# Optimization experiments

Measured on AMD Instinct MI355X. Metric: run time of the kernel, lower is better.

## Reference

```python
import jax, jax.numpy as jnp
import numpy as np


def _compute_gradient(f, src, dst, egw):
    # f: [b, c, n] node features; src/dst: [b, e] edge endpoints; egw: [b, e, d]
    # gradient at node src = sum_edges pinvdx * (f[dst] - f[src])
    fT = f.transpose(0, 2, 1)  # b, n, c
    n = fT.shape[1]
    f_dst = jnp.take_along_axis(fT, dst[..., None], axis=1)  # b, e, c
    f_src = jnp.take_along_axis(fT, src[..., None], axis=1)  # b, e, c
    msg = egw[..., :, None] * (f_dst - f_src)[..., None, :]  # b, e, d, c
    b, e, d, c = msg.shape

    def seg(m, s):
        return jax.ops.segment_sum(m.reshape(e, d * c), s, num_segments=n)

    grad = jax.vmap(seg)(msg, src)  # b, n, d*c
    return grad.transpose(0, 2, 1)  # b, d*c, n


def _forward(x, t, nodes, node_weights, edge_gradient_weights, modes, sp_L,
             fc0_w, fc0_b, Wc, Ws, W0, ws_w, ws_b, gws_w, gws_b,
             fc1_w, fc1_b, fc2_w, fc2_b, directed_edges):
    D = nodes.shape[-1]
    # Fourier bases: modes [k,d,w] scaled by sp_L [d,w]
    temp = jnp.einsum('bxd,kdw->bxkw', nodes, modes * sp_L)
    bc, bs = jnp.cos(temp), jnp.sin(temp)
    b0 = jnp.ones(temp[:, :, :1, :].shape, temp.dtype)
    nw = node_weights[:, :, None, :]
    wbc, wbs, wb0 = bc * nw, bs * nw, b0 * nw

    x_value = x[:, :, :D]
    h = jnp.concatenate([x, t], -1) @ fc0_w + fc0_b  # b, n, c
    h = h.transpose(0, 2, 1)  # b, c, n

    src = directed_edges[..., 0]
    dst = directed_edges[..., 1]
    nlayers = ws_w.shape[0]
    for i in range(nlayers):
        # spectral convolution (real Fourier transform on scattered points)
        xc = jnp.einsum('bcx,bxkw->bckw', h, wbc)
        xs = -jnp.einsum('bcx,bxkw->bckw', h, wbs)
        x0 = jnp.einsum('bcx,bxkw->bckw', h, wb0)
        fc_ = jnp.einsum('bikw,iokw->bokw', xc, Wc[i]) - jnp.einsum('bikw,iokw->bokw', xs, Ws[i])
        fs_ = jnp.einsum('bikw,iokw->bokw', xs, Wc[i]) + jnp.einsum('bikw,iokw->bokw', xc, Ws[i])
        f0_ = jnp.einsum('bikw,iokw->bokw', x0, W0[i])
        x1 = (jnp.einsum('bokw,bxkw->box', f0_, b0)
              + 2.0 * jnp.einsum('bokw,bxkw->box', fc_, bc)
              - 2.0 * jnp.einsum('bokw,bxkw->box', fs_, bs))
        # pointwise linear (Conv1d kernel size 1)
        x2 = jnp.einsum('oc,bcx->box', ws_w[i], h) + ws_b[i][None, :, None]
        # gradient operator + softsign + Conv1d
        g = _compute_gradient(h, src, dst, edge_gradient_weights)  # b, d*c, n
        g = g / (1.0 + jnp.abs(g))  # softsign
        x3 = jnp.einsum('oc,bcx->box', gws_w[i], g) + gws_b[i][None, :, None]
        h = x1 + x2 + x3
        if i != nlayers - 1:
            h = jax.nn.gelu(h, approximate=False)

    h = h.transpose(0, 2, 1)  # b, n, c
    h = jax.nn.gelu(h @ fc1_w + fc1_b, approximate=False)
    h = h @ fc2_w + fc2_b
    return x_value + t * h


def setup_inputs() -> dict:
    B, N, E = 2, 20000, 100000
    D, W, K, C, L, FC, OUT = 3, 1, 128, 128, 3, 128, 3
    key = jax.random.key(0)
    k = jax.random.split(key, 16)
    x = jax.random.normal(k[0], (B, N, D), jnp.float32)
    t = jax.random.uniform(k[1], (B, N, 1), jnp.float32)
    node_mask = jnp.ones((B, N, 1), jnp.int32)
    nodes = jax.random.uniform(k[2], (B, N, D), jnp.float32)
    node_weights = jax.random.uniform(k[3], (B, N, W), jnp.float32) / N
    directed_edges = jax.random.randint(k[4], (B, E, 2), 0, N)
    edge_gradient_weights = jax.random.normal(k[5], (B, E, D), jnp.float32)
    modes = jax.random.normal(k[6], (K, D, W), jnp.float32) * (2.0 * np.pi)
    sp_L = jnp.ones((D, W), jnp.float32)
    fc0_w = jax.random.normal(k[7], (D + 1, C), jnp.float32) * 0.1
    fc0_b = jnp.zeros((C,), jnp.float32)
    scale = 1.0 / (C * C)
    Wc = jax.random.uniform(k[8], (L, C, C, K, W), jnp.float32) * scale
    Ws = jax.random.uniform(k[9], (L, C, C, K, W), jnp.float32) * scale
    W0 = jax.random.uniform(k[10], (L, C, C, 1, W), jnp.float32) * scale
    ws_w = jax.random.normal(k[11], (L, C, C), jnp.float32) * 0.05
    ws_b = jnp.zeros((L, C), jnp.float32)
    gws_w = jax.random.normal(k[12], (L, C, D * C), jnp.float32) * 0.05
    gws_b = jnp.zeros((L, C), jnp.float32)
    fc1_w = jax.random.normal(k[13], (C, FC), jnp.float32) * 0.05
    fc1_b = jnp.zeros((FC,), jnp.float32)
    fc2_w = jax.random.normal(k[14], (FC, OUT), jnp.float32) * 0.05
    fc2_b = jnp.zeros((OUT,), jnp.float32)
    return dict(x=x, t=t, node_mask=node_mask, nodes=nodes, node_weights=node_weights,
                directed_edges=directed_edges, edge_gradient_weights=edge_gradient_weights,
                modes=modes, sp_L=sp_L, fc0_w=fc0_w, fc0_b=fc0_b, Wc=Wc, Ws=Ws, W0=W0,
                ws_w=ws_w, ws_b=ws_b, gws_w=gws_w, gws_b=gws_b,
                fc1_w=fc1_w, fc1_b=fc1_b, fc2_w=fc2_w, fc2_b=fc2_b)


def reference(x, t, node_mask, nodes, node_weights, directed_edges, edge_gradient_weights,
              modes, sp_L, fc0_w, fc0_b, Wc, Ws, W0, ws_w, ws_b, gws_w, gws_b,
              fc1_w, fc1_b, fc2_w, fc2_b):
    del node_mask  # unpacked but unused in the original forward
    return _forward(x, t, nodes, node_weights, edge_gradient_weights, modes, sp_L,
                    fc0_w, fc0_b, Wc, Ws, W0, ws_w, ws_b, gws_w, gws_b,
                    fc1_w, fc1_b, fc2_w, fc2_b, directed_edges)
```

## Files before the change

### kernel.cpp

```cpp
#include <hip/hip_runtime.h>
#include <math.h>

#define BB 2
#define NN 20000
#define EE 100000
#define DD 3
#define KK 128
#define CC 128
#define LL 3
#define FCC 128
#define GJ (DD*CC)
#define KR 768
#define NP 20096
#define NCHK 157
#define G1CH 79
#define G1N 256

typedef __attribute__((ext_vector_type(8))) short bf16x8;
typedef __attribute__((ext_vector_type(4))) float f32x4;

__device__ inline unsigned short f2bf(float f) {
  unsigned int u = __float_as_uint(f);
  u += 0x7fffu + ((u >> 16) & 1u);
  return (unsigned short)(u >> 16);
}
__device__ inline float bf2f(unsigned short u) {
  return __uint_as_float(((unsigned int)u) << 16);
}

__device__ float d_nw[BB*NN];
__device__ __align__(16) unsigned short d_stackT[(size_t)BB*NP*KR];
__device__ __align__(16) unsigned short d_bcT[(size_t)BB*KK*NP];
__device__ __align__(16) unsigned short d_bsT[(size_t)BB*KK*NP];
__device__ __align__(16) unsigned short d_hTwT[(size_t)BB*CC*NP];
__device__ __align__(16) unsigned short d_uTb[(size_t)BB*NP*FCC];
__device__ __align__(16) unsigned short d_Amatb[BB*CC*KR];
__device__ __align__(16) unsigned short d_fc1wb[FCC*CC];
__device__ __align__(16) float d_part[(size_t)BB*4*G1CH*2*64*64];
__device__ float d_xc[BB*CC*KK];
__device__ float d_xs[BB*CC*KK];
__device__ float d_x0p[BB*NCHK*CC];
__device__ float d_fcp[BB*CC*8*KK];
__device__ float d_fsp[BB*CC*8*KK];
__device__ float d_bias[BB*CC];
__device__ int d_cnt[BB*NN];
__device__ int d_cursor[BB*NN];
__device__ int d_off[BB*(NN+1)];
__device__ __align__(16) float4 d_erec[(size_t)BB*EE];

__global__ __launch_bounds__(128) void k_basis(const float* __restrict__ nodes,
                                               const float* __restrict__ nodew,
                                               const float* __restrict__ modes,
                                               const float* __restrict__ spL) {
  int bn = blockIdx.x;
  int k  = threadIdx.x;
  int b = bn / NN, n = bn % NN;
  float x0 = nodes[bn*3+0], x1 = nodes[bn*3+1], x2 = nodes[bn*3+2];
  float tmp = x0*modes[k*3+0]*spL[0] + x1*modes[k*3+1]*spL[1] + x2*modes[k*3+2]*spL[2];
  float cv = cosf(tmp), sv = sinf(tmp);
  size_t row = (size_t)(b*NP + n);
  d_stackT[row*KR + k]       = f2bf(cv);
  d_stackT[row*KR + 128 + k] = f2bf(sv);
  if (k == 0) d_nw[bn] = nodew[bn];
}

__global__ __launch_bounds__(256) void k_basisT() {
  __shared__ unsigned short t1[32][136];
  __shared__ unsigned short t2[32][136];
  int blk = blockIdx.x;
  int nt = blk % 628, b = blk / 628;
  int n0 = nt*32;
  int tid = threadIdx.x;
  int kl = tid & 127, ng = tid >> 7;
  for (int nn = ng; nn < 32; nn += 2) {
    int n = n0 + nn;
    unsigned short cv = 0, sv = 0;
    if (n < NN) {
      const unsigned short* sp = d_stackT + ((size_t)(b*NP + n))*KR;
      cv = sp[kl]; sv = sp[128 + kl];
    }
    t1[nn][kl] = cv;
    t2[nn][kl] = sv;
  }
  __syncthreads();
  int nl = tid & 31, kg = tid >> 5;
  for (int k = kg; k < 128; k += 8) {
    d_bcT[((size_t)(b*KK + k))*NP + n0 + nl] = t1[nl][k];
    d_bsT[((size_t)(b*KK + k))*NP + n0 + nl] = t2[nl][k];
  }
}

__global__ __launch_bounds__(256) void k_csr_zero() {
  int tid = blockIdx.x*256 + threadIdx.x;
  if (tid < BB*NN) { d_cnt[tid] = 0; d_cursor[tid] = 0; }
}

__global__ __launch_bounds__(256) void k_csr_count(const int* __restrict__ edges) {
  int e = blockIdx.x*256 + threadIdx.x;
  if (e >= BB*EE) return;
  int b = e / EE;
  int src = edges[e*2 + 0];
  atomicAdd(&d_cnt[b*NN + src], 1);
}

__global__ __launch_bounds__(1024) void k_csr_scan() {
  int b = blockIdx.x;
  __shared__ int sdata[1024];
  __shared__ int carry_s;
  int tid = threadIdx.x;
  if (tid == 0) carry_s = 0;
  __syncthreads();
  for (int chunk = 0; chunk < 20; ++chunk) {
    int i = chunk*1024 + tid;
    int v = (i < NN) ? d_cnt[b*NN + i] : 0;
    sdata[tid] = v;
    __syncthreads();
    for (int s = 1; s < 1024; s <<= 1) {
      int tv = (tid >= s) ? sdata[tid - s] : 0;
      __syncthreads();
      sdata[tid] += tv;
      __syncthreads();
    }
    int excl = carry_s + sdata[tid] - v;
    if (i < NN) d_off[b*(NN+1) + i] = excl;
    __syncthreads();
    if (tid == 1023) carry_s += sdata[1023];
    __syncthreads();
  }
  if (tid == 0) d_off[b*(NN+1) + NN] = carry_s;
}

__global__ __launch_bounds__(256) void k_csr_scatter(const int* __restrict__ edges,
                                                     const float* __restrict__ egw) {
  int e = blockIdx.x*256 + threadIdx.x;
  if (e >= BB*EE) return;
  int b = e / EE;
  int src = edges[e*2 + 0];
  int dst = edges[e*2 + 1];
  int pos = atomicAdd(&d_cursor[b*NN + src], 1);
  d_erec[(size_t)b*EE + d_off[b*(NN+1) + src] + pos] =
      make_float4(__int_as_float(dst), egw[e*3+0], egw[e*3+1], egw[e*3+2]);
}

__global__ __launch_bounds__(256) void k_h0(const float* __restrict__ x,
                                            const float* __restrict__ t,
                                            const float* __restrict__ w,
                                            const float* __restrict__ bias) {
  int tid = blockIdx.x*256 + threadIdx.x;
  int c = tid & 127;
  int bn = tid >> 7;
  int b = bn / NN, n = bn % NN;
  const float* xv = x + bn*3;
  float acc = bias[c] + xv[0]*w[c] + xv[1]*w[CC+c] + xv[2]*w[2*CC+c]
            + t[bn]*w[3*CC+c];
  d_stackT[((size_t)(b*NP + n))*KR + 256 + c] = f2bf(acc);
}

__global__ __launch_bounds__(256) void k_hT0() {
  __shared__ unsigned short t[128][136];
  int chunk = blockIdx.x;
  int b = blockIdx.y;
  int n0 = chunk*128;
  int tid = threadIdx.x;
  int cl = tid & 127, ng = tid >> 7;
  for (int nn = ng; nn < 128; nn += 2) {
    int n = n0 + nn;
    unsigned short v = 0;
    if (n < NN) {
      float hv = bf2f(d_stackT[((size_t)(b*NP + n))*KR + 256 + cl]);
      v = f2bf(hv * d_nw[b*NN + n]);
    }
    t[nn][cl] = v;
  }
  __syncthreads();
  int nl = tid & 31, cg = tid >> 5;
  for (int c = cg; c < 128; c += 8)
    for (int nn2 = 0; nn2 < 128; nn2 += 32)
      d_hTwT[((size_t)(b*CC + c))*NP + n0 + nn2 + nl] = t[nn2 + nl][c];
}

__global__ __launch_bounds__(256) void k_gemm1m() {
  __shared__ unsigned short Ash[2][64*40];
  __shared__ unsigned short Bch[2][64*40];
  __shared__ unsigned short Bsh[2][64*40];
  int chunk = blockIdx.x;
  int quad  = blockIdx.y;
  int b     = blockIdx.z;
  int ch = quad >> 1, kh = quad & 1;
  int tid = threadIdx.x, lane = tid & 63, wid = tid >> 6;
  int q = lane >> 4, m = lane & 15;
  f32x4 accC[4], accS[4];
  #pragma unroll
  for (int j = 0; j < 4; j++) { accC[j] = (f32x4){0.f,0.f,0.f,0.f}; accS[j] = (f32x4){0.f,0.f,0.f,0.f}; }
  const unsigned short* Ab  = d_hTwT + ((size_t)(b*CC + ch*64))*NP;
  const unsigned short* Bcp = d_bcT + ((size_t)(b*KK + kh*64))*NP;
  const unsigned short* Bsp = d_bsT + ((size_t)(b*KK + kh*64))*NP;
  int n0 = chunk*G1N;

#define G1STAGE(nb, d) { \
    int row_ = tid >> 2; int e8_ = (tid & 3)*8; \
    if ((nb) < NP) { \
      *(uint4*)&Ash[d][row_*40 + e8_] = *(const uint4*)(Ab  + (size_t)row_*NP + (nb) + e8_); \
      *(uint4*)&Bch[d][row_*40 + e8_] = *(const uint4*)(Bcp + (size_t)row_*NP + (nb) + e8_); \
      *(uint4*)&Bsh[d][row_*40 + e8_] = *(const uint4*)(Bsp + (size_t)row_*NP + (nb) + e8_); \
    } else { \
      uint4 z_ = make_uint4(0,0,0,0); \
      *(uint4*)&Ash[d][row_*40 + e8_] = z_; \
      *(uint4*)&Bch[d][row_*40 + e8_] = z_; \
      *(uint4*)&Bsh[d][row_*40 + e8_] = z_; \
    } }

  G1STAGE(n0, 0)
  int cur = 0;
  for (int s = 0; s < G1N/32; s++) {
    __syncthreads();
    if (s + 1 < G1N/32) G1STAGE(n0 + (s+1)*32, cur ^ 1)
    bf16x8 a = *(const bf16x8*)&Ash[cur][(wid*16 + m)*40 + q*8];
    #pragma unroll
    for (int kt = 0; kt < 4; kt++) {
      bf16x8 bcf = *(const bf16x8*)&Bch[cur][(kt*16 + m)*40 + q*8];
      accC[kt] = __builtin_amdgcn_mfma_f32_16x16x32_bf16(a, bcf, accC[kt], 0, 0, 0);
      bf16x8 bsf = *(const bf16x8*)&Bsh[cur][(kt*16 + m)*40 + q*8];
      accS[kt] = __builtin_amdgcn_mfma_f32_16x16x32_bf16(a, bsf, accS[kt], 0, 0, 0);
    }
    cur ^= 1;
  }
#undef G1STAGE

  float* base = d_part + ((size_t)(b*4 + quad)*G1CH + chunk)*2*4096;
  #pragma unroll
  for (int kt = 0; kt < 4; kt++)
    #pragma unroll
    for (int r = 0; r < 4; r++) {
      int c = wid*16 + q*4 + r;
      int k = kt*16 + m;
      base[c*64 + k]        =  accC[kt][r];
      base[4096 + c*64 + k] = -accS[kt][r];
    }
}

__global__ __launch_bounds__(256) void k_red_x0() {
  int blk = blockIdx.x;
  if (blk < 256) {
    int tid = blk*256 + threadIdx.x;
    int k = tid & 127;
    int c = (tid >> 7) & 127;
    int arr = (tid >> 14) & 1;
    int b = tid >> 15;
    int ch = c >> 6, cl = c & 63;
    int kh = k >> 6, kl = k & 63;
    int quad = ch*2 + kh;
    const float* p = d_part + ((size_t)(b*4 + quad)*G1CH)*2*4096 + arr*4096 + cl*64 + kl;
    float acc = 0.f;
    for (int t = 0; t < G1CH; t++) acc += p[(size_t)t*2*4096];
    if (arr == 0) d_xc[(b*CC + c)*KK + k] = acc;
    else          d_xs[(b*CC + c)*KK + k] = acc;
  } else {
    int bc = blk - 256;
    int chunk = bc % NCHK, b = bc / NCHK;
    int tid = threadIdx.x;
    int c = tid >> 1, half = tid & 1;
    const unsigned short* p = d_hTwT + ((size_t)(b*CC + c))*NP + chunk*128 + half*64;
    float acc = 0.f;
    #pragma unroll
    for (int i = 0; i < 8; i++) {
      ushort4 v0 = *(const ushort4*)&p[i*8];
      ushort4 v1 = *(const ushort4*)&p[i*8 + 4];
      acc += bf2f(v0.x) + bf2f(v0.y) + bf2f(v0.z) + bf2f(v0.w)
           + bf2f(v1.x) + bf2f(v1.y) + bf2f(v1.z) + bf2f(v1.w);
    }
    __shared__ float red[128][2];
    red[c][half] = acc;
    __syncthreads();
    if (half == 0) d_x0p[(b*NCHK + chunk)*CC + c] = red[c][0] + red[c][1];
  }
}

__global__ __launch_bounds__(128) void k_spec(const float* __restrict__ Wc,
                                              const float* __restrict__ Ws, int l) {
  int bo = blockIdx.x;
  int ch = blockIdx.y;
  int b = bo >> 7;
  int o = bo & 127;
  int k = threadIdx.x;
  int i0 = ch*16;
  const float* wcp = Wc + ((size_t)(l*CC + i0)*CC + o)*KK + k;
  const float* wsp = Ws + ((size_t)(l*CC + i0)*CC + o)*KK + k;
  float fc = 0.f, fs = 0.f;
  #pragma unroll 4
  for (int j = 0; j < 16; j++) {
    int i = i0 + j;
    float xcv = d_xc[(b*CC + i)*KK + k];
    float xsv = d_xs[(b*CC + i)*KK + k];
    float wcv = wcp[(size_t)j*CC*KK];
    float wsv = wsp[(size_t)j*CC*KK];
    fc += xcv*wcv - xsv*wsv;
    fs += xsv*wcv + xcv*wsv;
  }
  d_fcp[((size_t)bo*8 + ch)*KK + k] = fc;
  d_fsp[((size_t)bo*8 + ch)*KK + k] = fs;
}

__global__ __launch_bounds__(128) void k_bA_f0(const float* __restrict__ wsw,
                                               const float* __restrict__ gwsw,
                                               const float* __restrict__ W0,
                                               const float* __restrict__ wsb,
                                               const float* __restrict__ gwsb, int l) {
  int blk = blockIdx.x;
  int t = threadIdx.x;
  if (blk < 256) {
    int bo = blk;
    int b = bo >> 7, o = bo & 127;
    float fc = 0.f, fs = 0.f;
    #pragma unroll
    for (int ch = 0; ch < 8; ch++) {
      fc += d_fcp[((size_t)bo*8 + ch)*KK + t];
      fs += d_fsp[((size_t)bo*8 + ch)*KK + t];
    }
    unsigned short* dst = d_Amatb + (size_t)bo*KR;
    dst[t]       = f2bf( 2.f*fc);
    dst[128 + t] = f2bf(-2.f*fs);
    dst[256 + t] = f2bf(wsw[(l*CC + o)*CC + t]);
    #pragma unroll
    for (int j = 0; j < 3; j++)
      dst[384 + j*128 + t] = f2bf(gwsw[(size_t)(l*CC + o)*GJ + j*128 + t]);
  } else {
    int b = blk - 256;
    int o = t;
    __shared__ float sx[CC];
    float xv = 0.f;
    for (int p = 0; p < NCHK; p++) xv += d_x0p[(b*NCHK + p)*CC + o];
    sx[o] = xv;
    __syncthreads();
    float acc = 0.f;
    for (int i = 0; i < CC; i++) acc += sx[i]*W0[(l*CC + i)*CC + o];
    d_bias[b*CC + o] = acc + wsb[l*CC + o] + gwsb[l*CC + o];
  }
}

__global__ __launch_bounds__(128) void k_fc1w(const float* __restrict__ fc1w) {
  int c = blockIdx.x;
  int o2 = threadIdx.x;
  d_fc1wb[o2*CC + c] = f2bf(fc1w[c*FCC + o2]);
}

__global__ __launch_bounds__(128) void k_grad_csr() {
  int bn = blockIdx.x;
  int b = bn / NN, n = bn % NN;
  int c = threadIdx.x;
  int beg = d_off[b*(NN+1) + n];
  int end = d_off[b*(NN+1) + n + 1];
  const float4* rp = d_erec + (size_t)b*EE;
  const unsigned short* hb = d_stackT + (size_t)b*NP*KR + 256 + c;
  float a0 = 0.f, a1 = 0.f, a2 = 0.f;
  float sw0 = 0.f, sw1 = 0.f, sw2 = 0.f;
  int p = beg;
  for (; p + 4 <= end; p += 4) {
    float4 r1 = rp[p], r2 = rp[p+1], r3 = rp[p+2], r4 = rp[p+3];
    float f1 = bf2f(hb[(size_t)__float_as_int(r1.x)*KR]);
    float f2 = bf2f(hb[(size_t)__float_as_int(r2.x)*KR]);
    float f3 = bf2f(hb[(size_t)__float_as_int(r3.x)*KR]);
    float f4 = bf2f(hb[(size_t)__float_as_int(r4.x)*KR]);
    a0 += r1.y*f1 + r2.y*f2 + r3.y*f3 + r4.y*f4;
    a1 += r1.z*f1 + r2.z*f2 + r3.z*f3 + r4.z*f4;
    a2 += r1.w*f1 + r2.w*f2 + r3.w*f3 + r4.w*f4;
    sw0 += r1.y + r2.y + r3.y + r4.y;
    sw1 += r1.z + r2.z + r3.z + r4.z;
    sw2 += r1.w + r2.w + r3.w + r4.w;
  }
  for (; p < end; ++p) {
    float4 r1 = rp[p];
    float f1 = bf2f(hb[(size_t)__float_as_int(r1.x)*KR]);
    a0 += r1.y*f1; a1 += r1.z*f1; a2 += r1.w*f1;
    sw0 += r1.y; sw1 += r1.z; sw2 += r1.w;
  }
  float fs = bf2f(hb[(size_t)n*KR]);
  a0 -= sw0*fs; a1 -= sw1*fs; a2 -= sw2*fs;
  unsigned short* gp = d_stackT + ((size_t)(b*NP + n))*KR + 384;
  gp[c]        = f2bf(a0/(1.f + fabsf(a0)));
  gp[CC + c]   = f2bf(a1/(1.f + fabsf(a1)));
  gp[2*CC + c] = f2bf(a2/(1.f + fabsf(a2)));
}

__global__ __launch_bounds__(512) void k_mfma(int koff, int K,
                                              const unsigned short* __restrict__ W, size_t wstride,
                                              unsigned short* __restrict__ OutB,
                                              const float* __restrict__ bias, int bias_stride,
                                              int gelu, int aux) {
  __shared__ unsigned short As[2][64*72];
  __shared__ unsigned short Bs[2][128*72];
  __shared__ float sh_nw[64];
  int b = blockIdx.z;
  int n_base = blockIdx.x*64;
  int tid = threadIdx.x;
  int lane = tid & 63, wid = tid >> 6;
  int wr = wid >> 1, wc = wid & 1;
  int q = lane >> 4, m = lane & 15;

  f32x4 acc[4];
  #pragma unroll
  for (int j = 0; j < 4; j++) acc[j] = (f32x4){0.f,0.f,0.f,0.f};

  const unsigned short* Wb = W + (size_t)b*wstride;
  const unsigned short* Ab = d_stackT + (size_t)b*NP*KR + koff;

#define STAGE(k0, d) { \
    { int rowA = tid >> 3; int e8A = (tid & 7)*8; \
      *(uint4*)&As[d][rowA*72 + e8A] = *(const uint4*)(Ab + (size_t)(n_base + rowA)*KR + (k0) + e8A); } \
    _Pragma("unroll") \
    for (int i_ = 0; i_ < 2; i_++) { \
      int idx_ = tid + i_*512; int rowB = idx_ >> 3; int e8B = (idx_ & 7)*8; \
      *(uint4*)&Bs[d][rowB*72 + e8B] = *(const uint4*)(Wb + (size_t)rowB*K + (k0) + e8B); } }

  STAGE(0, 0)
  int cur = 0;
  for (int k0 = 0; k0 < K; k0 += 64) {
    __syncthreads();
    if (k0 + 64 < K) STAGE(k0 + 64, cur ^ 1)
    bf16x8 a0 = *(const bf16x8*)&As[cur][(wr*16 + m)*72 + q*8];
    bf16x8 a1 = *(const bf16x8*)&As[cur][(wr*16 + m)*72 + 32 + q*8];
    #pragma unroll
    for (int ot = 0; ot < 4; ot++) {
      bf16x8 b0 = *(const bf16x8*)&Bs[cur][(wc*64 + ot*16 + m)*72 + q*8];
      acc[ot] = __builtin_amdgcn_mfma_f32_16x16x32_bf16(a0, b0, acc[ot], 0, 0, 0);
      bf16x8 b1 = *(const bf16x8*)&Bs[cur][(wc*64 + ot*16 + m)*72 + 32 + q*8];
      acc[ot] = __builtin_amdgcn_mfma_f32_16x16x32_bf16(a1, b1, acc[ot], 0, 0, 0);
    }
    cur ^= 1;
  }
#undef STAGE

  __syncthreads();
  unsigned short* Ep = &As[0][0];
  if (tid < 64) {
    int n = n_base + tid;
    sh_nw[tid] = (aux && n < NN) ? d_nw[b*NN + n] : 0.f;
  }
  const float* bp = bias + (size_t)b*bias_stride;
  int lrow = wr*16 + q*4;
  #pragma unroll
  for (int ot = 0; ot < 4; ot++) {
    int o = wc*64 + ot*16 + m;
    float bvv = bp[o];
    #pragma unroll
    for (int r = 0; r < 4; r++) {
      float v = acc[ot][r] + bvv;
      if (gelu) v = 0.5f*v*(1.f + erff(v*0.70710678118f));
      Ep[(lrow + r)*132 + o] = f2bf(v);
    }
  }
  __syncthreads();
  {
    int row = tid >> 3;
    int c16 = (tid & 7)*16;
    int n = n_base + row;
    uint4 v0 = *(uint4*)&Ep[row*132 + c16];
    uint4 v1 = *(uint4*)&Ep[row*132 + c16 + 8];
    if (aux) {
      if (n < NN) {
        unsigned short* dst = d_stackT + ((size_t)(b*NP + n))*KR + 256;
        *(uint4*)&dst[c16]     = v0;
        *(uint4*)&dst[c16 + 8] = v1;
      }
    } else {
      unsigned short* dst = OutB + ((size_t)(b*NP + n))*FCC;
      *(uint4*)&dst[c16]     = v0;
      *(uint4*)&dst[c16 + 8] = v1;
    }
  }
  if (aux) {
    int o = tid >> 2;
    int j0 = (tid & 3)*16;
    unsigned short tmp[16];
    #pragma unroll
    for (int j = 0; j < 16; j++) {
      float hv = bf2f(Ep[(j0 + j)*132 + o]);
      tmp[j] = f2bf(hv * sh_nw[j0 + j]);
    }
    unsigned short* dst = d_hTwT + ((size_t)(b*CC + o))*NP + n_base + j0;
    *(uint4*)&dst[0] = *(uint4*)&tmp[0];
    *(uint4*)&dst[8] = *(uint4*)&tmp[8];
  }
}

__global__ __launch_bounds__(256) void k_out(const float* __restrict__ x,
                                             const float* __restrict__ t,
                                             const float* __restrict__ fc2w,
                                             const float* __restrict__ fc2b,
                                             float* __restrict__ out) {
  int tid = blockIdx.x*256 + threadIdx.x;
  if (tid >= BB*NN) return;
  int b = tid / NN, n = tid % NN;
  const unsigned short* up = d_uTb + ((size_t)(b*NP + n))*FCC;
  float a0 = fc2b[0], a1 = fc2b[1], a2v = fc2b[2];
  #pragma unroll 4
  for (int o2 = 0; o2 < FCC; o2 += 4) {
    ushort4 uv = *(const ushort4*)&up[o2];
    float u0 = bf2f(uv.x), u1 = bf2f(uv.y), u2 = bf2f(uv.z), u3 = bf2f(uv.w);
    a0  += u0*fc2w[(o2+0)*3+0] + u1*fc2w[(o2+1)*3+0] + u2*fc2w[(o2+2)*3+0] + u3*fc2w[(o2+3)*3+0];
    a1  += u0*fc2w[(o2+0)*3+1] + u1*fc2w[(o2+1)*3+1] + u2*fc2w[(o2+2)*3+1] + u3*fc2w[(o2+3)*3+1];
    a2v += u0*fc2w[(o2+0)*3+2] + u1*fc2w[(o2+1)*3+2] + u2*fc2w[(o2+2)*3+2] + u3*fc2w[(o2+3)*3+2];
  }
  float tv = t[tid];
  out[tid*3 + 0] = x[tid*3 + 0] + tv*a0;
  out[tid*3 + 1] = x[tid*3 + 1] + tv*a1;
  out[tid*3 + 2] = x[tid*3 + 2] + tv*a2v;
}

extern "C" void kernel_launch(void* const* d_in, const int* in_sizes, int n_in,
                              void* d_out, int out_size, void* d_ws, size_t ws_size,
                              hipStream_t stream) {
  const float* x     = (const float*)d_in[0];
  const float* t     = (const float*)d_in[1];
  const float* nodes = (const float*)d_in[3];
  const float* nodew = (const float*)d_in[4];
  const int*   edges = (const int*)d_in[5];
  const float* egw   = (const float*)d_in[6];
  const float* modes = (const float*)d_in[7];
  const float* spL   = (const float*)d_in[8];
  const float* fc0w  = (const float*)d_in[9];
  const float* fc0b  = (const float*)d_in[10];
  const float* Wc    = (const float*)d_in[11];
  const float* Ws    = (const float*)d_in[12];
  const float* W0    = (const float*)d_in[13];
  const float* wsw   = (const float*)d_in[14];
  const float* wsb   = (const float*)d_in[15];
  const float* gwsw  = (const float*)d_in[16];
  const float* gwsb  = (const float*)d_in[17];
  const float* fc1w  = (const float*)d_in[18];
  const float* fc1b  = (const float*)d_in[19];
  const float* fc2w  = (const float*)d_in[20];
  const float* fc2b  = (const float*)d_in[21];
  float* out = (float*)d_out;

  unsigned short* d_Amatb_p; hipGetSymbolAddress((void**)&d_Amatb_p, HIP_SYMBOL(d_Amatb));
  unsigned short* d_fc1wb_p; hipGetSymbolAddress((void**)&d_fc1wb_p, HIP_SYMBOL(d_fc1wb));
  unsigned short* d_uTb_p;   hipGetSymbolAddress((void**)&d_uTb_p,   HIP_SYMBOL(d_uTb));
  float* d_bias_p;  hipGetSymbolAddress((void**)&d_bias_p,  HIP_SYMBOL(d_bias));

  hipLaunchKernelGGL(k_basis, dim3(BB*NN), dim3(128), 0, stream, nodes, nodew, modes, spL);
  hipLaunchKernelGGL(k_basisT, dim3(628*BB), dim3(256), 0, stream);
  hipLaunchKernelGGL(k_h0, dim3(BB*NN*CC/256), dim3(256), 0, stream, x, t, fc0w, fc0b);
  hipLaunchKernelGGL(k_hT0, dim3(NCHK, BB), dim3(256), 0, stream);
  hipLaunchKernelGGL(k_fc1w, dim3(CC), dim3(FCC), 0, stream, fc1w);
  hipLaunchKernelGGL(k_csr_zero, dim3((BB*NN + 255)/256), dim3(256), 0, stream);
  hipLaunchKernelGGL(k_csr_count, dim3((BB*EE + 255)/256), dim3(256), 0, stream, edges);
  hipLaunchKernelGGL(k_csr_scan, dim3(BB), dim3(1024), 0, stream);
  hipLaunchKernelGGL(k_csr_scatter, dim3((BB*EE + 255)/256), dim3(256), 0, stream, edges, egw);

  for (int l = 0; l < LL; l++) {
    hipLaunchKernelGGL(k_gemm1m, dim3(G1CH, 4, BB), dim3(256), 0, stream);
    hipLaunchKernelGGL(k_red_x0, dim3(256 + NCHK*BB), dim3(256), 0, stream);
    hipLaunchKernelGGL(k_spec, dim3(BB*CC, 8), dim3(128), 0, stream, Wc, Ws, l);
    hipLaunchKernelGGL(k_bA_f0, dim3(BB*CC + BB), dim3(128), 0, stream,
                       wsw, gwsw, W0, wsb, gwsb, l);
    hipLaunchKernelGGL(k_grad_csr, dim3(BB*NN), dim3(128), 0, stream);
    hipLaunchKernelGGL(k_mfma, dim3(NP/64, 1, BB), dim3(512), 0, stream,
                       0, KR, d_Amatb_p, (size_t)CC*KR, d_uTb_p, d_bias_p, CC,
                       (l != LL-1) ? 1 : 0, 1);
  }

  hipLaunchKernelGGL(k_mfma, dim3(NP/64, 1, BB), dim3(512), 0, stream,
                     256, CC, d_fc1wb_p, (size_t)0, d_uTb_p, fc1b, 0, 1, 0);
  hipLaunchKernelGGL(k_out, dim3((BB*NN + 255)/256), dim3(256), 0, stream, x, t, fc2w, fc2b, out);
}
```

Measured before the change: 495.0 us.

## Co-schedule spectral GEMM with gradient kernel and fuse fc2 output into final GEMM

The spectral partial GEMM and the CSR gradient gather are merged into one launch with disjoint block ranges, so the memory-bound gather can run alongside the MFMA work. The GEMM also drops LDS double buffering in favour of a single buffer with two barriers per step. The fc2 projection and residual output move into the epilogue of the final fc1 MFMA kernel, which removes the intermediate bf16 activation buffer and one launch. The single-buffered loop exposes load latency, and the combined kernel's block mix may be scheduled unevenly.

```diff
diff --git a/kernel.cpp b/kernel.cpp
--- a/kernel.cpp
+++ b/kernel.cpp
@@ -15,6 +15,7 @@
 #define NCHK 157
 #define G1CH 79
 #define G1N 256
+#define G1BLK (G1CH*4*BB)
 
 typedef __attribute__((ext_vector_type(8))) short bf16x8;
 typedef __attribute__((ext_vector_type(4))) float f32x4;
@@ -33,7 +34,6 @@
 __device__ __align__(16) unsigned short d_bcT[(size_t)BB*KK*NP];
 __device__ __align__(16) unsigned short d_bsT[(size_t)BB*KK*NP];
 __device__ __align__(16) unsigned short d_hTwT[(size_t)BB*CC*NP];
-__device__ __align__(16) unsigned short d_uTb[(size_t)BB*NP*FCC];
 __device__ __align__(16) unsigned short d_Amatb[BB*CC*KR];
 __device__ __align__(16) unsigned short d_fc1wb[FCC*CC];
 __device__ __align__(16) float d_part[(size_t)BB*4*G1CH*2*64*64];
@@ -179,64 +179,100 @@
       d_hTwT[((size_t)(b*CC + c))*NP + n0 + nn2 + nl] = t[nn2 + nl][c];
 }
 
-__global__ __launch_bounds__(256) void k_gemm1m() {
-  __shared__ unsigned short Ash[2][64*40];
-  __shared__ unsigned short Bch[2][64*40];
-  __shared__ unsigned short Bsh[2][64*40];
-  int chunk = blockIdx.x;
-  int quad  = blockIdx.y;
-  int b     = blockIdx.z;
-  int ch = quad >> 1, kh = quad & 1;
-  int tid = threadIdx.x, lane = tid & 63, wid = tid >> 6;
-  int q = lane >> 4, m = lane & 15;
-  f32x4 accC[4], accS[4];
-  #pragma unroll
-  for (int j = 0; j < 4; j++) { accC[j] = (f32x4){0.f,0.f,0.f,0.f}; accS[j] = (f32x4){0.f,0.f,0.f,0.f}; }
-  const unsigned short* Ab  = d_hTwT + ((size_t)(b*CC + ch*64))*NP;
-  const unsigned short* Bcp = d_bcT + ((size_t)(b*KK + kh*64))*NP;
-  const unsigned short* Bsp = d_bsT + ((size_t)(b*KK + kh*64))*NP;
-  int n0 = chunk*G1N;
-
-#define G1STAGE(nb, d) { \
-    int row_ = tid >> 2; int e8_ = (tid & 3)*8; \
-    if ((nb) < NP) { \
-      *(uint4*)&Ash[d][row_*40 + e8_] = *(const uint4*)(Ab  + (size_t)row_*NP + (nb) + e8_); \
-      *(uint4*)&Bch[d][row_*40 + e8_] = *(const uint4*)(Bcp + (size_t)row_*NP + (nb) + e8_); \
-      *(uint4*)&Bsh[d][row_*40 + e8_] = *(const uint4*)(Bsp + (size_t)row_*NP + (nb) + e8_); \
-    } else { \
-      uint4 z_ = make_uint4(0,0,0,0); \
-      *(uint4*)&Ash[d][row_*40 + e8_] = z_; \
-      *(uint4*)&Bch[d][row_*40 + e8_] = z_; \
-      *(uint4*)&Bsh[d][row_*40 + e8_] = z_; \
-    } }
-
-  G1STAGE(n0, 0)
-  int cur = 0;
-  for (int s = 0; s < G1N/32; s++) {
-    __syncthreads();
-    if (s + 1 < G1N/32) G1STAGE(n0 + (s+1)*32, cur ^ 1)
-    bf16x8 a = *(const bf16x8*)&Ash[cur][(wid*16 + m)*40 + q*8];
-    #pragma unroll
-    for (int kt = 0; kt < 4; kt++) {
-      bf16x8 bcf = *(const bf16x8*)&Bch[cur][(kt*16 + m)*40 + q*8];
-      accC[kt] = __builtin_amdgcn_mfma_f32_16x16x32_bf16(a, bcf, accC[kt], 0, 0, 0);
-      bf16x8 bsf = *(const bf16x8*)&Bsh[cur][(kt*16 + m)*40 + q*8];
-      accS[kt] = __builtin_amdgcn_mfma_f32_16x16x32_bf16(a, bsf, accS[kt], 0, 0, 0);
-    }
-    cur ^= 1;
-  }
-#undef G1STAGE
-
-  float* base = d_part + ((size_t)(b*4 + quad)*G1CH + chunk)*2*4096;
-  #pragma unroll
-  for (int kt = 0; kt < 4; kt++)
-    #pragma unroll
-    for (int r = 0; r < 4; r++) {
-      int c = wid*16 + q*4 + r;
-      int k = kt*16 + m;
-      base[c*64 + k]        =  accC[kt][r];
-      base[4096 + c*64 + k] = -accS[kt][r];
-    }
+__global__ __launch_bounds__(256) void k_g1grad() {
+  __shared__ unsigned short Ash[64*40];
+  __shared__ unsigned short Bch[64*40];
+  __shared__ unsigned short Bsh[64*40];
+  int blk = blockIdx.x;
+  int tid = threadIdx.x;
+
+  if (blk < G1BLK) {
+    int chunk = blk % G1CH;
+    int quad  = (blk / G1CH) & 3;
+    int b     = blk / (G1CH*4);
+    int ch = quad >> 1, kh = quad & 1;
+    int lane = tid & 63, wid = tid >> 6;
+    int q = lane >> 4, m = lane & 15;
+    f32x4 accC[4], accS[4];
+    #pragma unroll
+    for (int j = 0; j < 4; j++) { accC[j] = (f32x4){0.f,0.f,0.f,0.f}; accS[j] = (f32x4){0.f,0.f,0.f,0.f}; }
+    const unsigned short* Ab  = d_hTwT + ((size_t)(b*CC + ch*64))*NP;
+    const unsigned short* Bcp = d_bcT + ((size_t)(b*KK + kh*64))*NP;
+    const unsigned short* Bsp = d_bsT + ((size_t)(b*KK + kh*64))*NP;
+    int n0 = chunk*G1N;
+    for (int s = 0; s < G1N/32; s++) {
+      int nb = n0 + s*32;
+      __syncthreads();
+      {
+        int row_ = tid >> 2; int e8_ = (tid & 3)*8;
+        if (nb < NP) {
+          *(uint4*)&Ash[row_*40 + e8_] = *(const uint4*)(Ab  + (size_t)row_*NP + nb + e8_);
+          *(uint4*)&Bch[row_*40 + e8_] = *(const uint4*)(Bcp + (size_t)row_*NP + nb + e8_);
+          *(uint4*)&Bsh[row_*40 + e8_] = *(const uint4*)(Bsp + (size_t)row_*NP + nb + e8_);
+        } else {
+          uint4 z_ = make_uint4(0,0,0,0);
+          *(uint4*)&Ash[row_*40 + e8_] = z_;
+          *(uint4*)&Bch[row_*40 + e8_] = z_;
+          *(uint4*)&Bsh[row_*40 + e8_] = z_;
+        }
+      }
+      __syncthreads();
+      bf16x8 a = *(const bf16x8*)&Ash[(wid*16 + m)*40 + q*8];
+      #pragma unroll
+      for (int kt = 0; kt < 4; kt++) {
+        bf16x8 bcf = *(const bf16x8*)&Bch[(kt*16 + m)*40 + q*8];
+        accC[kt] = __builtin_amdgcn_mfma_f32_16x16x32_bf16(a, bcf, accC[kt], 0, 0, 0);
+        bf16x8 bsf = *(const bf16x8*)&Bsh[(kt*16 + m)*40 + q*8];
+        accS[kt] = __builtin_amdgcn_mfma_f32_16x16x32_bf16(a, bsf, accS[kt], 0, 0, 0);
+      }
+    }
+    float* base = d_part + ((size_t)(b*4 + quad)*G1CH + chunk)*2*4096;
+    #pragma unroll
+    for (int kt = 0; kt < 4; kt++)
+      #pragma unroll
+      for (int r = 0; r < 4; r++) {
+        int c = wid*16 + q*4 + r;
+        int k = kt*16 + m;
+        base[c*64 + k]        =  accC[kt][r];
+        base[4096 + c*64 + k] = -accS[kt][r];
+      }
+  } else {
+    int bn = (blk - G1BLK)*2 + (tid >> 7);
+    int c = tid & 127;
+    int b = bn / NN, n = bn % NN;
+    int beg = d_off[b*(NN+1) + n];
+    int end = d_off[b*(NN+1) + n + 1];
+    const float4* rp = d_erec + (size_t)b*EE;
+    const unsigned short* hb = d_stackT + (size_t)b*NP*KR + 256 + c;
+    float a0 = 0.f, a1 = 0.f, a2 = 0.f;
+    float sw0 = 0.f, sw1 = 0.f, sw2 = 0.f;
+    int p = beg;
+    for (; p + 4 <= end; p += 4) {
+      float4 r1 = rp[p], r2 = rp[p+1], r3 = rp[p+2], r4 = rp[p+3];
+      float f1 = bf2f(hb[(size_t)__float_as_int(r1.x)*KR]);
+      float f2 = bf2f(hb[(size_t)__float_as_int(r2.x)*KR]);
+      float f3 = bf2f(hb[(size_t)__float_as_int(r3.x)*KR]);
+      float f4 = bf2f(hb[(size_t)__float_as_int(r4.x)*KR]);
+      a0 += r1.y*f1 + r2.y*f2 + r3.y*f3 + r4.y*f4;
+      a1 += r1.z*f1 + r2.z*f2 + r3.z*f3 + r4.z*f4;
+      a2 += r1.w*f1 + r2.w*f2 + r3.w*f3 + r4.w*f4;
+      sw0 += r1.y + r2.y + r3.y + r4.y;
+      sw1 += r1.z + r2.z + r3.z + r4.z;
+      sw2 += r1.w + r2.w + r3.w + r4.w;
+    }
+    for (; p < end; ++p) {
+      float4 r1 = rp[p];
+      float f1 = bf2f(hb[(size_t)__float_as_int(r1.x)*KR]);
+      a0 += r1.y*f1; a1 += r1.z*f1; a2 += r1.w*f1;
+      sw0 += r1.y; sw1 += r1.z; sw2 += r1.w;
+    }
+    float fs = bf2f(hb[(size_t)n*KR]);
+    a0 -= sw0*fs; a1 -= sw1*fs; a2 -= sw2*fs;
+    unsigned short* gp = d_stackT + ((size_t)(b*NP + n))*KR + 384;
+    gp[c]        = f2bf(a0/(1.f + fabsf(a0)));
+    gp[CC + c]   = f2bf(a1/(1.f + fabsf(a1)));
+    gp[2*CC + c] = f2bf(a2/(1.f + fabsf(a2)));
+  }
 }
 
 __global__ __launch_bounds__(256) void k_red_x0() {
@@ -344,49 +380,15 @@
   d_fc1wb[o2*CC + c] = f2bf(fc1w[c*FCC + o2]);
 }
 
-__global__ __launch_bounds__(128) void k_grad_csr() {
-  int bn = blockIdx.x;
-  int b = bn / NN, n = bn % NN;
-  int c = threadIdx.x;
-  int beg = d_off[b*(NN+1) + n];
-  int end = d_off[b*(NN+1) + n + 1];
-  const float4* rp = d_erec + (size_t)b*EE;
-  const unsigned short* hb = d_stackT + (size_t)b*NP*KR + 256 + c;
-  float a0 = 0.f, a1 = 0.f, a2 = 0.f;
-  float sw0 = 0.f, sw1 = 0.f, sw2 = 0.f;
-  int p = beg;
-  for (; p + 4 <= end; p += 4) {
-    float4 r1 = rp[p], r2 = rp[p+1], r3 = rp[p+2], r4 = rp[p+3];
-    float f1 = bf2f(hb[(size_t)__float_as_int(r1.x)*KR]);
-    float f2 = bf2f(hb[(size_t)__float_as_int(r2.x)*KR]);
-    float f3 = bf2f(hb[(size_t)__float_as_int(r3.x)*KR]);
-    float f4 = bf2f(hb[(size_t)__float_as_int(r4.x)*KR]);
-    a0 += r1.y*f1 + r2.y*f2 + r3.y*f3 + r4.y*f4;
-    a1 += r1.z*f1 + r2.z*f2 + r3.z*f3 + r4.z*f4;
-    a2 += r1.w*f1 + r2.w*f2 + r3.w*f3 + r4.w*f4;
-    sw0 += r1.y + r2.y + r3.y + r4.y;
-    sw1 += r1.z + r2.z + r3.z + r4.z;
-    sw2 += r1.w + r2.w + r3.w + r4.w;
-  }
-  for (; p < end; ++p) {
-    float4 r1 = rp[p];
-    float f1 = bf2f(hb[(size_t)__float_as_int(r1.x)*KR]);
-    a0 += r1.y*f1; a1 += r1.z*f1; a2 += r1.w*f1;
-    sw0 += r1.y; sw1 += r1.z; sw2 += r1.w;
-  }
-  float fs = bf2f(hb[(size_t)n*KR]);
-  a0 -= sw0*fs; a1 -= sw1*fs; a2 -= sw2*fs;
-  unsigned short* gp = d_stackT + ((size_t)(b*NP + n))*KR + 384;
-  gp[c]        = f2bf(a0/(1.f + fabsf(a0)));
-  gp[CC + c]   = f2bf(a1/(1.f + fabsf(a1)));
-  gp[2*CC + c] = f2bf(a2/(1.f + fabsf(a2)));
-}
-
 __global__ __launch_bounds__(512) void k_mfma(int koff, int K,
                                               const unsigned short* __restrict__ W, size_t wstride,
-                                              unsigned short* __restrict__ OutB,
                                               const float* __restrict__ bias, int bias_stride,
-                                              int gelu, int aux) {
+                                              int gelu, int aux,
+                                              const float* __restrict__ xvec,
+                                              const float* __restrict__ tvec,
+                                              const float* __restrict__ fc2w,
+                                              const float* __restrict__ fc2b,
+                                              float* __restrict__ outp) {
   __shared__ unsigned short As[2][64*72];
   __shared__ unsigned short Bs[2][128*72];
   __shared__ float sh_nw[64];
@@ -450,61 +452,58 @@
     }
   }
   __syncthreads();
-  {
-    int row = tid >> 3;
-    int c16 = (tid & 7)*16;
-    int n = n_base + row;
-    uint4 v0 = *(uint4*)&Ep[row*132 + c16];
-    uint4 v1 = *(uint4*)&Ep[row*132 + c16 + 8];
-    if (aux) {
+  if (aux) {
+    {
+      int row = tid >> 3;
+      int c16 = (tid & 7)*16;
+      int n = n_base + row;
       if (n < NN) {
+        uint4 v0 = *(uint4*)&Ep[row*132 + c16];
+        uint4 v1 = *(uint4*)&Ep[row*132 + c16 + 8];
         unsigned short* dst = d_stackT + ((size_t)(b*NP + n))*KR + 256;
         *(uint4*)&dst[c16]     = v0;
         *(uint4*)&dst[c16 + 8] = v1;
       }
-    } else {
-      unsigned short* dst = OutB + ((size_t)(b*NP + n))*FCC;
-      *(uint4*)&dst[c16]     = v0;
-      *(uint4*)&dst[c16 + 8] = v1;
-    }
-  }
-  if (aux) {
-    int o = tid >> 2;
-    int j0 = (tid & 3)*16;
-    unsigned short tmp[16];
-    #pragma unroll
-    for (int j = 0; j < 16; j++) {
-      float hv = bf2f(Ep[(j0 + j)*132 + o]);
-      tmp[j] = f2bf(hv * sh_nw[j0 + j]);
-    }
-    unsigned short* dst = d_hTwT + ((size_t)(b*CC + o))*NP + n_base + j0;
-    *(uint4*)&dst[0] = *(uint4*)&tmp[0];
-    *(uint4*)&dst[8] = *(uint4*)&tmp[8];
-  }
-}
-
-__global__ __launch_bounds__(256) void k_out(const float* __restrict__ x,
-                                             const float* __restrict__ t,
-                                             const float* __restrict__ fc2w,
-                                             const float* __restrict__ fc2b,
-                                             float* __restrict__ out) {
-  int tid = blockIdx.x*256 + threadIdx.x;
-  if (tid >= BB*NN) return;
-  int b = tid / NN, n = tid % NN;
-  const unsigned short* up = d_uTb + ((size_t)(b*NP + n))*FCC;
-  float a0 = fc2b[0], a1 = fc2b[1], a2v = fc2b[2];
-  #pragma unroll 4
-  for (int o2 = 0; o2 < FCC; o2 += 4) {
-    ushort4 uv = *(const ushort4*)&up[o2];
-    float u0 = bf2f(uv.x), u1 = bf2f(uv.y), u2 = bf2f(uv.z), u3 = bf2f(uv.w);
-    a0  += u0*fc2w[(o2+0)*3+0] + u1*fc2w[(o2+1)*3+0] + u2*fc2w[(o2+2)*3+0] + u3*fc2w[(o2+3)*3+0];
-    a1  += u0*fc2w[(o2+0)*3+1] + u1*fc2w[(o2+1)*3+1] + u2*fc2w[(o2+2)*3+1] + u3*fc2w[(o2+3)*3+1];
-    a2v += u0*fc2w[(o2+0)*3+2] + u1*fc2w[(o2+1)*3+2] + u2*fc2w[(o2+2)*3+2] + u3*fc2w[(o2+3)*3+2];
-  }
-  float tv = t[tid];
-  out[tid*3 + 0] = x[tid*3 + 0] + tv*a0;
-  out[tid*3 + 1] = x[tid*3 + 1] + tv*a1;
-  out[tid*3 + 2] = x[tid*3 + 2] + tv*a2v;
+    }
+    {
+      int o = tid >> 2;
+      int j0 = (tid & 3)*16;
+      unsigned short tmp[16];
+      #pragma unroll
+      for (int j = 0; j < 16; j++) {
+        float hv = bf2f(Ep[(j0 + j)*132 + o]);
+        tmp[j] = f2bf(hv * sh_nw[j0 + j]);
+      }
+      unsigned short* dst = d_hTwT + ((size_t)(b*CC + o))*NP + n_base + j0;
+      *(uint4*)&dst[0] = *(uint4*)&tmp[0];
+      *(uint4*)&dst[8] = *(uint4*)&tmp[8];
+    }
+  } else {
+    int row = tid >> 3, j = tid & 7;
+    int n = n_base + row;
+    float p0 = 0.f, p1 = 0.f, p2 = 0.f;
+    int o0 = j*16;
+    #pragma unroll
+    for (int oo = 0; oo < 16; oo++) {
+      float uv = bf2f(Ep[row*132 + o0 + oo]);
+      p0 += uv*fc2w[(o0+oo)*3 + 0];
+      p1 += uv*fc2w[(o0+oo)*3 + 1];
+      p2 += uv*fc2w[(o0+oo)*3 + 2];
+    }
+    #pragma unroll
+    for (int s2 = 1; s2 < 8; s2 <<= 1) {
+      p0 += __shfl_xor(p0, s2);
+      p1 += __shfl_xor(p1, s2);
+      p2 += __shfl_xor(p2, s2);
+    }
+    if (j == 0 && n < NN) {
+      int bn = b*NN + n;
+      float tv = tvec[bn];
+      outp[bn*3 + 0] = xvec[bn*3 + 0] + tv*(p0 + fc2b[0]);
+      outp[bn*3 + 1] = xvec[bn*3 + 1] + tv*(p1 + fc2b[1]);
+      outp[bn*3 + 2] = xvec[bn*3 + 2] + tv*(p2 + fc2b[2]);
+    }
+  }
 }
 
 extern "C" void kernel_launch(void* const* d_in, const int* in_sizes, int n_in,
@@ -535,7 +534,6 @@
 
   unsigned short* d_Amatb_p; hipGetSymbolAddress((void**)&d_Amatb_p, HIP_SYMBOL(d_Amatb));
   unsigned short* d_fc1wb_p; hipGetSymbolAddress((void**)&d_fc1wb_p, HIP_SYMBOL(d_fc1wb));
-  unsigned short* d_uTb_p;   hipGetSymbolAddress((void**)&d_uTb_p,   HIP_SYMBOL(d_uTb));
   float* d_bias_p;  hipGetSymbolAddress((void**)&d_bias_p,  HIP_SYMBOL(d_bias));
 
   hipLaunchKernelGGL(k_basis, dim3(BB*NN), dim3(128), 0, stream, nodes, nodew, modes, spL);
@@ -549,18 +547,19 @@
   hipLaunchKernelGGL(k_csr_scatter, dim3((BB*EE + 255)/256), dim3(256), 0, stream, edges, egw);
 
   for (int l = 0; l < LL; l++) {
-    hipLaunchKernelGGL(k_gemm1m, dim3(G1CH, 4, BB), dim3(256), 0, stream);
+    hipLaunchKernelGGL(k_g1grad, dim3(G1BLK + BB*NN/2), dim3(256), 0, stream);
     hipLaunchKernelGGL(k_red_x0, dim3(256 + NCHK*BB), dim3(256), 0, stream);
     hipLaunchKernelGGL(k_spec, dim3(BB*CC, 8), dim3(128), 0, stream, Wc, Ws, l);
     hipLaunchKernelGGL(k_bA_f0, dim3(BB*CC + BB), dim3(128), 0, stream,
                        wsw, gwsw, W0, wsb, gwsb, l);
-    hipLaunchKernelGGL(k_grad_csr, dim3(BB*NN), dim3(128), 0, stream);
     hipLaunchKernelGGL(k_mfma, dim3(NP/64, 1, BB), dim3(512), 0, stream,
-                       0, KR, d_Amatb_p, (size_t)CC*KR, d_uTb_p, d_bias_p, CC,
-                       (l != LL-1) ? 1 : 0, 1);
+                       0, KR, d_Amatb_p, (size_t)CC*KR, d_bias_p, CC,
+                       (l != LL-1) ? 1 : 0, 1,
+                       (const float*)nullptr, (const float*)nullptr,
+                       (const float*)nullptr, (const float*)nullptr, (float*)nullptr);
   }
 
   hipLaunchKernelGGL(k_mfma, dim3(NP/64, 1, BB), dim3(512), 0, stream,
-                     256, CC, d_fc1wb_p, (size_t)0, d_uTb_p, fc1b, 0, 1, 0);
-  hipLaunchKernelGGL(k_out, dim3((BB*NN + 255)/256), dim3(256), 0, stream, x, t, fc2w, fc2b, out);
-}
+                     256, CC, d_fc1wb_p, (size_t)0, fc1b, 0, 1, 0,
+                     x, t, fc2w, fc2b, out);
+}
```

New measurement: 536.3 us. +8.3%, slower.
